# Kernel tuning notes

Measured on AMD Instinct MI355X. Metric: run time of the kernel, lower is better.

Reference implementation:

```python
import jax, jax.numpy as jnp
import numpy as np

N_NODES = 100000
N_EDGES = 1600000
IN_CH, HID, OUT_CH = 512, 32, 64


def setup_inputs() -> dict:
    key = jax.random.key(0)
    ks = jax.random.split(key, 8)
    x = jax.random.normal(ks[0], (N_NODES, IN_CH), dtype=jnp.float32)
    edge_index = jax.random.randint(ks[1], (2, N_EDGES), 0, N_NODES, dtype=jnp.int64)
    def glorot(k, fan_in, fan_out):
        lim = np.sqrt(6.0 / (fan_in + fan_out)).astype(np.float32)
        return jax.random.uniform(k, (fan_in, fan_out), jnp.float32, -lim, lim)
    return {
        "x": x,
        "edge_index": edge_index,
        "W1": glorot(ks[2], IN_CH, HID), "b1": jnp.zeros((HID,), jnp.float32),
        "W2": glorot(ks[3], HID, HID),   "b2": jnp.zeros((HID,), jnp.float32),
        "W3": glorot(ks[4], HID, OUT_CH),"b3": jnp.zeros((OUT_CH,), jnp.float32),
    }


def _gcn_norm(edge_index, n_nodes):
    # PyG GCNConv: add self-loops, symmetric normalization D^-1/2 (A+I) D^-1/2
    loops = jnp.arange(n_nodes, dtype=edge_index.dtype)
    src = jnp.concatenate([edge_index[0], loops])
    dst = jnp.concatenate([edge_index[1], loops])
    deg = jax.ops.segment_sum(jnp.ones_like(dst, dtype=jnp.float32), dst,
                              num_segments=n_nodes)
    dinv = jnp.where(deg > 0, jax.lax.rsqrt(deg), 0.0)
    norm = dinv[src] * dinv[dst]  # [E + N]
    return src, dst, norm


def _gcn_conv(x, W, b, src, dst, norm, n_nodes):
    h = x @ W                                  # [N, F_out] dense GEMM
    msg = h[src] * norm[:, None]               # gather + scale over edges
    out = jax.ops.segment_sum(msg, dst, num_segments=n_nodes)  # scatter-add
    return out + b


def reference(x, edge_index, W1, b1, W2, b2, W3, b3):
    n = x.shape[0]
    src, dst, norm = _gcn_norm(edge_index, n)
    h = _gcn_conv(x, W1, b1, src, dst, norm, n)
    h = jax.nn.relu(h)  # dropout is identity in eval mode (training=False)
    h = _gcn_conv(h, W2, b2, src, dst, norm, n)
    h = jax.nn.relu(h)
    h = _gcn_conv(h, W3, b3, src, dst, norm, n)
    return jax.nn.log_softmax(h, axis=1)
```

## Files before the change

### kernel.cpp

```cpp
#include <hip/hip_runtime.h>
#include <math.h>

static constexpr int NN    = 100000;
static constexpr int NBUCK = (NN + 255) / 256;

#define CDIV(a,b) (((a)+(b)-1)/(b))

__device__ __forceinline__ float bf2f(unsigned short u) {
    return __uint_as_float(((unsigned)u) << 16);
}
__device__ __forceinline__ unsigned short f2bf(float f) {
    unsigned u = __float_as_uint(f);
    u += 0x7fffu + ((u >> 16) & 1u);
    return (unsigned short)(u >> 16);
}

__global__ __launch_bounds__(512) void k_zero(int* __restrict__ p, int n) {
    int i = blockIdx.x * 512 + threadIdx.x;
    if (i < n) p[i] = 0;
}

__global__ __launch_bounds__(256) void k_bcount(const int* __restrict__ dst,
                                                int* __restrict__ bcnt,
                                                int E, int chunk) {
    __shared__ int lc[NBUCK];
    for (int i = threadIdx.x; i < NBUCK; i += 256) lc[i] = 0;
    __syncthreads();
    int e0 = blockIdx.x * chunk;
    int e1 = e0 + chunk; if (e1 > E) e1 = E;
    for (int e = e0 + threadIdx.x; e < e1; e += 256)
        atomicAdd(&lc[dst[e] >> 8], 1);
    __syncthreads();
    for (int i = threadIdx.x; i < NBUCK; i += 256)
        if (lc[i]) atomicAdd(&bcnt[i], lc[i]);
}

__global__ __launch_bounds__(512) void k_bscan(const int* __restrict__ bcnt,
                                               int* __restrict__ bbase,
                                               int* __restrict__ bfill, int E) {
    __shared__ int sm[512];
    int t = threadIdx.x;
    int v = (t < NBUCK) ? bcnt[t] : 0;
    sm[t] = v; __syncthreads();
    for (int off = 1; off < 512; off <<= 1) {
        int u = (t >= off) ? sm[t - off] : 0;
        __syncthreads();
        sm[t] += u;
        __syncthreads();
    }
    if (t < NBUCK) { int ex = sm[t] - v; bbase[t] = ex; bfill[t] = ex; }
    if (t == 0) bbase[NBUCK] = E;
}

__global__ __launch_bounds__(256) void k_bpart(const int* __restrict__ src,
                                               const int* __restrict__ dst,
                                               int* __restrict__ bfill,
                                               unsigned int* __restrict__ part,
                                               int E, int chunk) {
    __shared__ int lc[NBUCK];
    __shared__ int boff[NBUCK];
    for (int i = threadIdx.x; i < NBUCK; i += 256) lc[i] = 0;
    __syncthreads();
    int e0 = blockIdx.x * chunk;
    int e1 = e0 + chunk; if (e1 > E) e1 = E;
    for (int e = e0 + threadIdx.x; e < e1; e += 256)
        atomicAdd(&lc[dst[e] >> 8], 1);
    __syncthreads();
    for (int i = threadIdx.x; i < NBUCK; i += 256) {
        int c = lc[i];
        boff[i] = c ? atomicAdd(&bfill[i], c) : 0;
        lc[i] = 0;
    }
    __syncthreads();
    for (int e = e0 + threadIdx.x; e < e1; e += 256) {
        int d = dst[e];
        int b = d >> 8;
        int pos = boff[b] + atomicAdd(&lc[b], 1);
        part[pos] = ((unsigned)src[e] << 8) | (unsigned)(d & 255);
    }
}

__global__ __launch_bounds__(256) void k_bbuild(const unsigned int* __restrict__ part,
                                                const int* __restrict__ bbase,
                                                int* __restrict__ row_ptr,
                                                float* __restrict__ dinv,
                                                int* __restrict__ col, int n, int E) {
    __shared__ int hist[256];
    __shared__ int excl[256];
    __shared__ int fill[256];
    const int b = blockIdx.x;
    const int t = threadIdx.x;
    const int e0 = bbase[b], e1 = bbase[b + 1];
    hist[t] = 0; fill[t] = 0;
    __syncthreads();
    for (int e = e0 + t; e < e1; e += 256)
        atomicAdd(&hist[part[e] & 255], 1);
    __syncthreads();
    int v = hist[t];
    excl[t] = v; __syncthreads();
    for (int off = 1; off < 256; off <<= 1) {
        int u = (t >= off) ? excl[t - off] : 0;
        __syncthreads();
        excl[t] += u;
        __syncthreads();
    }
    int ex = excl[t] - v;
    int g = b * 256 + t;
    if (g < n) {
        row_ptr[g] = e0 + ex;
        dinv[g] = rsqrtf((float)(v + 1));
    }
    if (b == 0 && t == 0) row_ptr[n] = E;
    excl[t] = e0 + ex;
    __syncthreads();
    for (int e = e0 + t; e < e1; e += 256) {
        unsigned u = part[e];
        int ld = u & 255;
        int pos = excl[ld] + atomicAdd(&fill[ld], 1);
        col[pos] = (int)(u >> 8);
    }
}

__global__ __launch_bounds__(256) void k_gemm1(const float* __restrict__ X,
                                               const float* __restrict__ W,
                                               const float* __restrict__ dinv,
                                               unsigned short* __restrict__ OUT,
                                               int nrows) {
    constexpr int K    = 512;
    constexpr int NOUT = 32;
    constexpr int KC   = 32;
    constexpr int RPB  = 64;
    constexpr int XST  = KC + 4;
    __shared__ float xs[2][RPB][XST];
    __shared__ float ws[2][KC][NOUT];

    const int t     = threadIdx.x;
    const int c0    = (t % 8) * 4;
    const int slot  = t / 8;
    const int grow0 = blockIdx.x * RPB;
    const int srow  = t / 8;
    const int skq   = t % 8;

    float acc[2][4] = {{0.f,0.f,0.f,0.f},{0.f,0.f,0.f,0.f}};

    auto clampRow = [&](int lrow) {
        int rr = grow0 + lrow;
        return (rr > nrows - 1) ? (nrows - 1) : rr;
    };
    const float* xrowA = X + (size_t)clampRow(srow) * K;
    const float* xrowB = X + (size_t)clampRow(32 + srow) * K;

    {
        float4 a = *(const float4*)&xrowA[skq * 4];
        float4 b = *(const float4*)&xrowB[skq * 4];
        float4 w = *(const float4*)&W[(size_t)srow * NOUT + skq * 4];
        *(float4*)&xs[0][srow][skq * 4]      = a;
        *(float4*)&xs[0][32 + srow][skq * 4] = b;
        *(float4*)&ws[0][srow][skq * 4]      = w;
    }
    __syncthreads();

    int buf = 0;
    const int r0 = slot * 2;
    for (int kc = 0; kc < K; kc += KC) {
        const bool more = (kc + KC < K);
        float4 pa, pb, pw;
        if (more) {
            pa = *(const float4*)&xrowA[kc + KC + skq * 4];
            pb = *(const float4*)&xrowB[kc + KC + skq * 4];
            pw = *(const float4*)&W[(size_t)(kc + KC + srow) * NOUT + skq * 4];
        }
        #pragma unroll
        for (int k = 0; k < KC; k += 4) {
            float4 x0 = *(const float4*)&xs[buf][r0][k];
            float4 x1 = *(const float4*)&xs[buf][r0 + 1][k];
            float4 w0 = *(const float4*)&ws[buf][k + 0][c0];
            float4 w1 = *(const float4*)&ws[buf][k + 1][c0];
            float4 w2 = *(const float4*)&ws[buf][k + 2][c0];
            float4 w3 = *(const float4*)&ws[buf][k + 3][c0];
            acc[0][0] += x0.x*w0.x + x0.y*w1.x + x0.z*w2.x + x0.w*w3.x;
            acc[0][1] += x0.x*w0.y + x0.y*w1.y + x0.z*w2.y + x0.w*w3.y;
            acc[0][2] += x0.x*w0.z + x0.y*w1.z + x0.z*w2.z + x0.w*w3.z;
            acc[0][3] += x0.x*w0.w + x0.y*w1.w + x0.z*w2.w + x0.w*w3.w;
            acc[1][0] += x1.x*w0.x + x1.y*w1.x + x1.z*w2.x + x1.w*w3.x;
            acc[1][1] += x1.x*w0.y + x1.y*w1.y + x1.z*w2.y + x1.w*w3.y;
            acc[1][2] += x1.x*w0.z + x1.y*w1.z + x1.z*w2.z + x1.w*w3.z;
            acc[1][3] += x1.x*w0.w + x1.y*w1.w + x1.z*w2.w + x1.w*w3.w;
        }
        if (more) {
            *(float4*)&xs[buf ^ 1][srow][skq * 4]      = pa;
            *(float4*)&xs[buf ^ 1][32 + srow][skq * 4] = pb;
            *(float4*)&ws[buf ^ 1][srow][skq * 4]      = pw;
            __syncthreads();
            buf ^= 1;
        }
    }
    #pragma unroll
    for (int r = 0; r < 2; r++) {
        int rr = grow0 + r0 + r;
        if (rr < nrows) {
            float d = dinv[rr];
            ushort4 o;
            o.x = f2bf(acc[r][0] * d); o.y = f2bf(acc[r][1] * d);
            o.z = f2bf(acc[r][2] * d); o.w = f2bf(acc[r][3] * d);
            *(ushort4*)&OUT[(size_t)rr * NOUT + c0] = o;
        }
    }
}

__device__ __forceinline__ float4 agg_gather_bf16(const unsigned short* __restrict__ HS,
                                                  const int* __restrict__ col,
                                                  int s0, int s1, int node, int c0) {
    float4 a0 = {0,0,0,0}, a1 = {0,0,0,0}, a2 = {0,0,0,0}, a3 = {0,0,0,0};
    int e = s0;
    for (; e + 3 < s1; e += 4) {
        int sA = col[e], sB = col[e + 1], sC = col[e + 2], sD = col[e + 3];
        ushort4 uA = *(const ushort4*)&HS[(size_t)sA * 32 + c0];
        ushort4 uB = *(const ushort4*)&HS[(size_t)sB * 32 + c0];
        ushort4 uC = *(const ushort4*)&HS[(size_t)sC * 32 + c0];
        ushort4 uD = *(const ushort4*)&HS[(size_t)sD * 32 + c0];
        a0.x += bf2f(uA.x); a0.y += bf2f(uA.y); a0.z += bf2f(uA.z); a0.w += bf2f(uA.w);
        a1.x += bf2f(uB.x); a1.y += bf2f(uB.y); a1.z += bf2f(uB.z); a1.w += bf2f(uB.w);
        a2.x += bf2f(uC.x); a2.y += bf2f(uC.y); a2.z += bf2f(uC.z); a2.w += bf2f(uC.w);
        a3.x += bf2f(uD.x); a3.y += bf2f(uD.y); a3.z += bf2f(uD.z); a3.w += bf2f(uD.w);
    }
    for (; e < s1; e++) {
        int sA = col[e];
        ushort4 uA = *(const ushort4*)&HS[(size_t)sA * 32 + c0];
        a0.x += bf2f(uA.x); a0.y += bf2f(uA.y); a0.z += bf2f(uA.z); a0.w += bf2f(uA.w);
    }
    ushort4 uS = *(const ushort4*)&HS[(size_t)node * 32 + c0];
    float4 acc;
    acc.x = a0.x + a1.x + a2.x + a3.x + bf2f(uS.x);
    acc.y = a0.y + a1.y + a2.y + a3.y + bf2f(uS.y);
    acc.z = a0.z + a1.z + a2.z + a3.z + bf2f(uS.z);
    acc.w = a0.w + a1.w + a2.w + a3.w + bf2f(uS.w);
    return acc;
}

__global__ __launch_bounds__(256) void k_fuse32(const unsigned short* __restrict__ HS,
                                                const int* __restrict__ row_ptr,
                                                const int* __restrict__ col,
                                                const float* __restrict__ dinv,
                                                const float* __restrict__ bin,
                                                const float* __restrict__ W,
                                                unsigned short* __restrict__ OUT, int n) {
    __shared__ float ws[32][32];
    {
        int i = threadIdx.x;
        int r = i / 8, c = (i % 8) * 4;
        *(float4*)&ws[r][c] = *(const float4*)&W[r * 32 + c];
    }
    __syncthreads();
    const int t    = threadIdx.x;
    const int node = blockIdx.x * 32 + t / 8;
    const int c0   = (t % 8) * 4;
    if (node >= n) return;
    const int s0 = row_ptr[node], s1 = row_ptr[node + 1];
    float4 acc = agg_gather_bf16(HS, col, s0, s1, node, c0);
    const float di = dinv[node];
    float4 b4 = *(const float4*)&bin[c0];
    float4 a;
    a.x = fmaxf(di * acc.x + b4.x, 0.f);
    a.y = fmaxf(di * acc.y + b4.y, 0.f);
    a.z = fmaxf(di * acc.z + b4.z, 0.f);
    a.w = fmaxf(di * acc.w + b4.w, 0.f);
    float4 o = {0,0,0,0};
    const int gb = (t & 63) & ~7;
    #pragma unroll
    for (int s = 0; s < 8; s++) {
        float4 as;
        as.x = __shfl(a.x, gb + s, 64);
        as.y = __shfl(a.y, gb + s, 64);
        as.z = __shfl(a.z, gb + s, 64);
        as.w = __shfl(a.w, gb + s, 64);
        const int k0 = s * 4;
        float4 w0 = *(const float4*)&ws[k0 + 0][c0];
        float4 w1 = *(const float4*)&ws[k0 + 1][c0];
        float4 w2 = *(const float4*)&ws[k0 + 2][c0];
        float4 w3 = *(const float4*)&ws[k0 + 3][c0];
        o.x += as.x*w0.x + as.y*w1.x + as.z*w2.x + as.w*w3.x;
        o.y += as.x*w0.y + as.y*w1.y + as.z*w2.y + as.w*w3.y;
        o.z += as.x*w0.z + as.y*w1.z + as.z*w2.z + as.w*w3.z;
        o.w += as.x*w0.w + as.y*w1.w + as.z*w2.w + as.w*w3.w;
    }
    ushort4 st;
    st.x = f2bf(o.x * di); st.y = f2bf(o.y * di);
    st.z = f2bf(o.z * di); st.w = f2bf(o.w * di);
    *(ushort4*)&OUT[(size_t)node * 32 + c0] = st;
}

__global__ __launch_bounds__(256) void k_aggscale(const unsigned short* __restrict__ HS,
                                                  const int* __restrict__ row_ptr,
                                                  const int* __restrict__ col,
                                                  const float* __restrict__ dinv,
                                                  const float* __restrict__ bin,
                                                  unsigned short* __restrict__ OUT, int n) {
    const int t    = threadIdx.x;
    const int node = blockIdx.x * 32 + t / 8;
    const int c0   = (t % 8) * 4;
    if (node >= n) return;
    const int s0 = row_ptr[node], s1 = row_ptr[node + 1];
    float4 acc = agg_gather_bf16(HS, col, s0, s1, node, c0);
    const float di = dinv[node];
    float4 b4 = *(const float4*)&bin[c0];
    ushort4 o;
    o.x = f2bf(di * fmaxf(di * acc.x + b4.x, 0.f));
    o.y = f2bf(di * fmaxf(di * acc.y + b4.y, 0.f));
    o.z = f2bf(di * fmaxf(di * acc.z + b4.z, 0.f));
    o.w = f2bf(di * fmaxf(di * acc.w + b4.w, 0.f));
    *(ushort4*)&OUT[(size_t)node * 32 + c0] = o;
}

__global__ __launch_bounds__(256) void k_fuseC(const unsigned short* __restrict__ YS,
                                               const int* __restrict__ row_ptr,
                                               const int* __restrict__ col,
                                               const float* __restrict__ dinv,
                                               const float* __restrict__ b3,
                                               const float* __restrict__ W,
                                               float* __restrict__ OUT, int n) {
    __shared__ float ws[32][64];
    {
        int i = threadIdx.x;
        int r0w = i / 16, cw = (i % 16) * 4;
        *(float4*)&ws[r0w][cw]      = *(const float4*)&W[r0w * 64 + cw];
        *(float4*)&ws[r0w + 16][cw] = *(const float4*)&W[(r0w + 16) * 64 + cw];
    }
    __syncthreads();
    const int t    = threadIdx.x;
    const int node = blockIdx.x * 32 + t / 8;
    const int c0   = (t % 8) * 4;
    if (node >= n) return;
    const int s0 = row_ptr[node], s1 = row_ptr[node + 1];
    float4 acc = agg_gather_bf16(YS, col, s0, s1, node, c0);
    const float di = dinv[node];
    float4 g;
    g.x = di * acc.x; g.y = di * acc.y; g.z = di * acc.z; g.w = di * acc.w;
    float4 oL = {0,0,0,0}, oH = {0,0,0,0};
    const int gb = (t & 63) & ~7;
    #pragma unroll
    for (int s = 0; s < 8; s++) {
        float4 gs;
        gs.x = __shfl(g.x, gb + s, 64);
        gs.y = __shfl(g.y, gb + s, 64);
        gs.z = __shfl(g.z, gb + s, 64);
        gs.w = __shfl(g.w, gb + s, 64);
        const int k0 = s * 4;
        #pragma unroll
        for (int q = 0; q < 4; q++) {
            float gv = (q == 0) ? gs.x : (q == 1) ? gs.y : (q == 2) ? gs.z : gs.w;
            float4 wL = *(const float4*)&ws[k0 + q][c0];
            float4 wH = *(const float4*)&ws[k0 + q][32 + c0];
            oL.x += gv * wL.x; oL.y += gv * wL.y; oL.z += gv * wL.z; oL.w += gv * wL.w;
            oH.x += gv * wH.x; oH.y += gv * wH.y; oH.z += gv * wH.z; oH.w += gv * wH.w;
        }
    }
    float4 bL = *(const float4*)&b3[c0];
    float4 bH = *(const float4*)&b3[32 + c0];
    oL.x += bL.x; oL.y += bL.y; oL.z += bL.z; oL.w += bL.w;
    oH.x += bH.x; oH.y += bH.y; oH.z += bH.z; oH.w += bH.w;
    float m = fmaxf(fmaxf(fmaxf(oL.x, oL.y), fmaxf(oL.z, oL.w)),
                    fmaxf(fmaxf(oH.x, oH.y), fmaxf(oH.z, oH.w)));
    #pragma unroll
    for (int off = 1; off < 8; off <<= 1) m = fmaxf(m, __shfl_xor(m, off, 64));
    float sum = expf(oL.x - m) + expf(oL.y - m) + expf(oL.z - m) + expf(oL.w - m)
              + expf(oH.x - m) + expf(oH.y - m) + expf(oH.z - m) + expf(oH.w - m);
    #pragma unroll
    for (int off = 1; off < 8; off <<= 1) sum += __shfl_xor(sum, off, 64);
    float lse = m + logf(sum);
    float4 rL, rH;
    rL.x = oL.x - lse; rL.y = oL.y - lse; rL.z = oL.z - lse; rL.w = oL.w - lse;
    rH.x = oH.x - lse; rH.y = oH.y - lse; rH.z = oH.z - lse; rH.w = oH.w - lse;
    *(float4*)&OUT[(size_t)node * 64 + c0]      = rL;
    *(float4*)&OUT[(size_t)node * 64 + 32 + c0] = rH;
}

extern "C" void kernel_launch(void* const* d_in, const int* in_sizes, int n_in,
                              void* d_out, int out_size, void* d_ws, size_t ws_size,
                              hipStream_t stream) {
    const float* x  = (const float*)d_in[0];
    const int*   ei = (const int*)d_in[1];
    const float* W1 = (const float*)d_in[2];
    const float* b1 = (const float*)d_in[3];
    const float* W2 = (const float*)d_in[4];
    const float* b2 = (const float*)d_in[5];
    const float* W3 = (const float*)d_in[6];
    const float* b3 = (const float*)d_in[7];
    float* out = (float*)d_out;

    const int E = in_sizes[1] / 2;
    const int n = NN;
    const int* src = ei;
    const int* dst = ei + E;

    char* p = (char*)d_ws;
    auto alloc = [&](size_t bytes) -> void* {
        void* r = p;
        p += (bytes + 63) & ~(size_t)63;
        return r;
    };
    int*            bcnt    = (int*)alloc((size_t)NBUCK * 4);
    int*            bbase   = (int*)alloc((size_t)(NBUCK + 1) * 4);
    int*            bfill   = (int*)alloc((size_t)NBUCK * 4);
    unsigned*       part    = (unsigned*)alloc((size_t)E * 4);
    int*            row_ptr = (int*)alloc((size_t)(n + 1) * 4);
    int*            col     = (int*)alloc((size_t)E * 4);
    float*          dinv    = (float*)alloc((size_t)n * 4);
    unsigned short* hs1     = (unsigned short*)alloc((size_t)n * 32 * 2);
    unsigned short* hs2     = (unsigned short*)alloc((size_t)n * 32 * 2);

    const int NBLK_A = 256;
    const int chunk  = CDIV(E, NBLK_A);

    k_zero<<<1, 512, 0, stream>>>(bcnt, NBUCK);
    k_bcount<<<NBLK_A, 256, 0, stream>>>(dst, bcnt, E, chunk);
    k_bscan<<<1, 512, 0, stream>>>(bcnt, bbase, bfill, E);
    k_bpart<<<NBLK_A, 256, 0, stream>>>(src, dst, bfill, part, E, chunk);
    k_bbuild<<<NBUCK, 256, 0, stream>>>(part, bbase, row_ptr, dinv, col, n, E);

    k_gemm1<<<CDIV(n, 64), 256, 0, stream>>>(x, W1, dinv, hs1, n);
    k_fuse32<<<CDIV(n, 32), 256, 0, stream>>>(hs1, row_ptr, col, dinv, b1, W2, hs2, n);
    k_aggscale<<<CDIV(n, 32), 256, 0, stream>>>(hs2, row_ptr, col, dinv, b2, hs1, n);
    k_fuseC<<<CDIV(n, 32), 256, 0, stream>>>(hs1, row_ptr, col, dinv, b3, W3, out, n);
}
```

Baseline: 223.2 us.

## Use direct global-to-LDS loads in GEMM1 and 16-byte gathers in aggregation

The first GEMM now stages X and W tiles with global_load_lds straight into shared memory. It drops the register round-trip and the padded stride, and uses an XOR-style rotated column swizzle to avoid bank conflicts. The three aggregation kernels switch from 4 lanes of 8-byte bf16 loads per node to 4 threads per node each doing 16-byte gathers. This halves the lanes per node and doubles the nodes per block. The aim is fewer memory instructions per gathered row and less staging overhead, at the cost of more registers per thread and a swizzle that must match the LDS write pattern exactly.

After: 233.5 us. 4.6% more time.

```diff
diff --git a/kernel.cpp b/kernel.cpp
--- a/kernel.cpp
+++ b/kernel.cpp
@@ -6,13 +6,13 @@
 
 #define CDIV(a,b) (((a)+(b)-1)/(b))
 
-__device__ __forceinline__ float bf2f(unsigned short u) {
-    return __uint_as_float(((unsigned)u) << 16);
-}
 __device__ __forceinline__ unsigned short f2bf(float f) {
     unsigned u = __float_as_uint(f);
     u += 0x7fffu + ((u >> 16) & 1u);
     return (unsigned short)(u >> 16);
+}
+__device__ __forceinline__ unsigned packbf(float lo, float hi) {
+    return (unsigned)f2bf(lo) | ((unsigned)f2bf(hi) << 16);
 }
 
 __global__ __launch_bounds__(512) void k_zero(int* __restrict__ p, int n) {
@@ -130,8 +130,7 @@
     constexpr int NOUT = 32;
     constexpr int KC   = 32;
     constexpr int RPB  = 64;
-    constexpr int XST  = KC + 4;
-    __shared__ float xs[2][RPB][XST];
+    __shared__ float xs[2][RPB][KC];
     __shared__ float ws[2][KC][NOUT];
 
     const int t     = threadIdx.x;
@@ -140,6 +139,7 @@
     const int grow0 = blockIdx.x * RPB;
     const int srow  = t / 8;
     const int skq   = t % 8;
+    const int wid8  = (t >> 6) * 8;
 
     float acc[2][4] = {{0.f,0.f,0.f,0.f},{0.f,0.f,0.f,0.f}};
 
@@ -147,33 +147,36 @@
         int rr = grow0 + lrow;
         return (rr > nrows - 1) ? (nrows - 1) : rr;
     };
-    const float* xrowA = X + (size_t)clampRow(srow) * K;
-    const float* xrowB = X + (size_t)clampRow(32 + srow) * K;
-
-    {
-        float4 a = *(const float4*)&xrowA[skq * 4];
-        float4 b = *(const float4*)&xrowB[skq * 4];
-        float4 w = *(const float4*)&W[(size_t)srow * NOUT + skq * 4];
-        *(float4*)&xs[0][srow][skq * 4]      = a;
-        *(float4*)&xs[0][32 + srow][skq * 4] = b;
-        *(float4*)&ws[0][srow][skq * 4]      = w;
-    }
+    const int scol = ((skq - ((srow >> 1) & 7)) & 7) * 4;
+    const float* xrowA = X + (size_t)clampRow(srow) * K + scol;
+    const float* xrowB = X + (size_t)clampRow(32 + srow) * K + scol;
+
+    auto stage = [&](int bf, int kc) {
+        __builtin_amdgcn_global_load_lds(
+            (const __attribute__((address_space(1))) void*)(xrowA + kc),
+            (__attribute__((address_space(3))) void*)&xs[bf][wid8][0], 16, 0, 0);
+        __builtin_amdgcn_global_load_lds(
+            (const __attribute__((address_space(1))) void*)(xrowB + kc),
+            (__attribute__((address_space(3))) void*)&xs[bf][32 + wid8][0], 16, 0, 0);
+        __builtin_amdgcn_global_load_lds(
+            (const __attribute__((address_space(1))) void*)(W + (size_t)(kc + srow) * NOUT + skq * 4),
+            (__attribute__((address_space(3))) void*)&ws[bf][wid8][0], 16, 0, 0);
+    };
+
+    stage(0, 0);
     __syncthreads();
 
     int buf = 0;
     const int r0 = slot * 2;
+    const int q4 = (slot & 7) * 4;
     for (int kc = 0; kc < K; kc += KC) {
         const bool more = (kc + KC < K);
-        float4 pa, pb, pw;
-        if (more) {
-            pa = *(const float4*)&xrowA[kc + KC + skq * 4];
-            pb = *(const float4*)&xrowB[kc + KC + skq * 4];
-            pw = *(const float4*)&W[(size_t)(kc + KC + srow) * NOUT + skq * 4];
-        }
+        if (more) stage(buf ^ 1, kc + KC);
         #pragma unroll
         for (int k = 0; k < KC; k += 4) {
-            float4 x0 = *(const float4*)&xs[buf][r0][k];
-            float4 x1 = *(const float4*)&xs[buf][r0 + 1][k];
+            const int kq = (k + q4) & 31;
+            float4 x0 = *(const float4*)&xs[buf][r0][kq];
+            float4 x1 = *(const float4*)&xs[buf][r0 + 1][kq];
             float4 w0 = *(const float4*)&ws[buf][k + 0][c0];
             float4 w1 = *(const float4*)&ws[buf][k + 1][c0];
             float4 w2 = *(const float4*)&ws[buf][k + 2][c0];
@@ -187,13 +190,8 @@
             acc[1][2] += x1.x*w0.z + x1.y*w1.z + x1.z*w2.z + x1.w*w3.z;
             acc[1][3] += x1.x*w0.w + x1.y*w1.w + x1.z*w2.w + x1.w*w3.w;
         }
-        if (more) {
-            *(float4*)&xs[buf ^ 1][srow][skq * 4]      = pa;
-            *(float4*)&xs[buf ^ 1][32 + srow][skq * 4] = pb;
-            *(float4*)&ws[buf ^ 1][srow][skq * 4]      = pw;
-            __syncthreads();
-            buf ^= 1;
-        }
+        __syncthreads();
+        if (more) buf ^= 1;
     }
     #pragma unroll
     for (int r = 0; r < 2; r++) {
@@ -208,34 +206,42 @@
     }
 }
 
-__device__ __forceinline__ float4 agg_gather_bf16(const unsigned short* __restrict__ HS,
-                                                  const int* __restrict__ col,
-                                                  int s0, int s1, int node, int c0) {
-    float4 a0 = {0,0,0,0}, a1 = {0,0,0,0}, a2 = {0,0,0,0}, a3 = {0,0,0,0};
+__device__ __forceinline__ void acc8(float* a, uint4 u) {
+    a[0] += __uint_as_float(u.x << 16);
+    a[1] += __uint_as_float(u.x & 0xffff0000u);
+    a[2] += __uint_as_float(u.y << 16);
+    a[3] += __uint_as_float(u.y & 0xffff0000u);
+    a[4] += __uint_as_float(u.z << 16);
+    a[5] += __uint_as_float(u.z & 0xffff0000u);
+    a[6] += __uint_as_float(u.w << 16);
+    a[7] += __uint_as_float(u.w & 0xffff0000u);
+}
+
+__device__ __forceinline__ void agg_gather8(const unsigned short* __restrict__ HS,
+                                            const int* __restrict__ col,
+                                            int s0, int s1, int node, int c0h,
+                                            float* __restrict__ out) {
+    float a0[8], a1[8], a2[8], a3[8];
+    #pragma unroll
+    for (int j = 0; j < 8; j++) { a0[j] = a1[j] = a2[j] = a3[j] = 0.f; }
+    const char* base = (const char*)HS + (size_t)c0h * 2;
     int e = s0;
     for (; e + 3 < s1; e += 4) {
         int sA = col[e], sB = col[e + 1], sC = col[e + 2], sD = col[e + 3];
-        ushort4 uA = *(const ushort4*)&HS[(size_t)sA * 32 + c0];
-        ushort4 uB = *(const ushort4*)&HS[(size_t)sB * 32 + c0];
-        ushort4 uC = *(const ushort4*)&HS[(size_t)sC * 32 + c0];
-        ushort4 uD = *(const ushort4*)&HS[(size_t)sD * 32 + c0];
-        a0.x += bf2f(uA.x); a0.y += bf2f(uA.y); a0.z += bf2f(uA.z); a0.w += bf2f(uA.w);
-        a1.x += bf2f(uB.x); a1.y += bf2f(uB.y); a1.z += bf2f(uB.z); a1.w += bf2f(uB.w);
-        a2.x += bf2f(uC.x); a2.y += bf2f(uC.y); a2.z += bf2f(uC.z); a2.w += bf2f(uC.w);
-        a3.x += bf2f(uD.x); a3.y += bf2f(uD.y); a3.z += bf2f(uD.z); a3.w += bf2f(uD.w);
+        uint4 uA = *(const uint4*)(base + (size_t)sA * 64);
+        uint4 uB = *(const uint4*)(base + (size_t)sB * 64);
+        uint4 uC = *(const uint4*)(base + (size_t)sC * 64);
+        uint4 uD = *(const uint4*)(base + (size_t)sD * 64);
+        acc8(a0, uA); acc8(a1, uB); acc8(a2, uC); acc8(a3, uD);
     }
     for (; e < s1; e++) {
-        int sA = col[e];
-        ushort4 uA = *(const ushort4*)&HS[(size_t)sA * 32 + c0];
-        a0.x += bf2f(uA.x); a0.y += bf2f(uA.y); a0.z += bf2f(uA.z); a0.w += bf2f(uA.w);
-    }
-    ushort4 uS = *(const ushort4*)&HS[(size_t)node * 32 + c0];
-    float4 acc;
-    acc.x = a0.x + a1.x + a2.x + a3.x + bf2f(uS.x);
-    acc.y = a0.y + a1.y + a2.y + a3.y + bf2f(uS.y);
-    acc.z = a0.z + a1.z + a2.z + a3.z + bf2f(uS.z);
-    acc.w = a0.w + a1.w + a2.w + a3.w + bf2f(uS.w);
-    return acc;
+        uint4 uA = *(const uint4*)(base + (size_t)col[e] * 64);
+        acc8(a0, uA);
+    }
+    uint4 uS = *(const uint4*)(base + (size_t)node * 64);
+    acc8(a1, uS);
+    #pragma unroll
+    for (int j = 0; j < 8; j++) out[j] = (a0[j] + a1[j]) + (a2[j] + a3[j]);
 }
 
 __global__ __launch_bounds__(256) void k_fuse32(const unsigned short* __restrict__ HS,
@@ -253,41 +259,37 @@
     }
     __syncthreads();
     const int t    = threadIdx.x;
-    const int node = blockIdx.x * 32 + t / 8;
-    const int c0   = (t % 8) * 4;
+    const int node = blockIdx.x * 64 + t / 4;
+    const int c0h  = (t % 4) * 8;
     if (node >= n) return;
     const int s0 = row_ptr[node], s1 = row_ptr[node + 1];
-    float4 acc = agg_gather_bf16(HS, col, s0, s1, node, c0);
+    float acc[8];
+    agg_gather8(HS, col, s0, s1, node, c0h, acc);
     const float di = dinv[node];
-    float4 b4 = *(const float4*)&bin[c0];
-    float4 a;
-    a.x = fmaxf(di * acc.x + b4.x, 0.f);
-    a.y = fmaxf(di * acc.y + b4.y, 0.f);
-    a.z = fmaxf(di * acc.z + b4.z, 0.f);
-    a.w = fmaxf(di * acc.w + b4.w, 0.f);
-    float4 o = {0,0,0,0};
-    const int gb = (t & 63) & ~7;
-    #pragma unroll
-    for (int s = 0; s < 8; s++) {
-        float4 as;
-        as.x = __shfl(a.x, gb + s, 64);
-        as.y = __shfl(a.y, gb + s, 64);
-        as.z = __shfl(a.z, gb + s, 64);
-        as.w = __shfl(a.w, gb + s, 64);
-        const int k0 = s * 4;
-        float4 w0 = *(const float4*)&ws[k0 + 0][c0];
-        float4 w1 = *(const float4*)&ws[k0 + 1][c0];
-        float4 w2 = *(const float4*)&ws[k0 + 2][c0];
-        float4 w3 = *(const float4*)&ws[k0 + 3][c0];
-        o.x += as.x*w0.x + as.y*w1.x + as.z*w2.x + as.w*w3.x;
-        o.y += as.x*w0.y + as.y*w1.y + as.z*w2.y + as.w*w3.y;
-        o.z += as.x*w0.z + as.y*w1.z + as.z*w2.z + as.w*w3.z;
-        o.w += as.x*w0.w + as.y*w1.w + as.z*w2.w + as.w*w3.w;
-    }
-    ushort4 st;
-    st.x = f2bf(o.x * di); st.y = f2bf(o.y * di);
-    st.z = f2bf(o.z * di); st.w = f2bf(o.w * di);
-    *(ushort4*)&OUT[(size_t)node * 32 + c0] = st;
+    float a[8];
+    #pragma unroll
+    for (int j = 0; j < 8; j++)
+        a[j] = fmaxf(di * acc[j] + bin[c0h + j], 0.f);
+    float o[8] = {0,0,0,0,0,0,0,0};
+    const int gb = (t & 63) & ~3;
+    #pragma unroll
+    for (int s = 0; s < 4; s++) {
+        #pragma unroll
+        for (int j = 0; j < 8; j++) {
+            float av = __shfl(a[j], gb + s, 64);
+            const int kr = s * 8 + j;
+            float4 w0 = *(const float4*)&ws[kr][c0h];
+            float4 w1 = *(const float4*)&ws[kr][c0h + 4];
+            o[0] += av * w0.x; o[1] += av * w0.y; o[2] += av * w0.z; o[3] += av * w0.w;
+            o[4] += av * w1.x; o[5] += av * w1.y; o[6] += av * w1.z; o[7] += av * w1.w;
+        }
+    }
+    uint4 st;
+    st.x = packbf(o[0] * di, o[1] * di);
+    st.y = packbf(o[2] * di, o[3] * di);
+    st.z = packbf(o[4] * di, o[5] * di);
+    st.w = packbf(o[6] * di, o[7] * di);
+    *(uint4*)&OUT[(size_t)node * 32 + c0h] = st;
 }
 
 __global__ __launch_bounds__(256) void k_aggscale(const unsigned short* __restrict__ HS,
@@ -297,19 +299,23 @@
                                                   const float* __restrict__ bin,
                                                   unsigned short* __restrict__ OUT, int n) {
     const int t    = threadIdx.x;
-    const int node = blockIdx.x * 32 + t / 8;
-    const int c0   = (t % 8) * 4;
+    const int node = blockIdx.x * 64 + t / 4;
+    const int c0h  = (t % 4) * 8;
     if (node >= n) return;
     const int s0 = row_ptr[node], s1 = row_ptr[node + 1];
-    float4 acc = agg_gather_bf16(HS, col, s0, s1, node, c0);
+    float acc[8];
+    agg_gather8(HS, col, s0, s1, node, c0h, acc);
     const float di = dinv[node];
-    float4 b4 = *(const float4*)&bin[c0];
-    ushort4 o;
-    o.x = f2bf(di * fmaxf(di * acc.x + b4.x, 0.f));
-    o.y = f2bf(di * fmaxf(di * acc.y + b4.y, 0.f));
-    o.z = f2bf(di * fmaxf(di * acc.z + b4.z, 0.f));
-    o.w = f2bf(di * fmaxf(di * acc.w + b4.w, 0.f));
-    *(ushort4*)&OUT[(size_t)node * 32 + c0] = o;
+    float o[8];
+    #pragma unroll
+    for (int j = 0; j < 8; j++)
+        o[j] = di * fmaxf(di * acc[j] + bin[c0h + j], 0.f);
+    uint4 st;
+    st.x = packbf(o[0], o[1]);
+    st.y = packbf(o[2], o[3]);
+    st.z = packbf(o[4], o[5]);
+    st.w = packbf(o[6], o[7]);
+    *(uint4*)&OUT[(size_t)node * 32 + c0h] = st;
 }
 
 __global__ __launch_bounds__(256) void k_fuseC(const unsigned short* __restrict__ YS,
@@ -328,51 +334,58 @@
     }
     __syncthreads();
     const int t    = threadIdx.x;
-    const int node = blockIdx.x * 32 + t / 8;
-    const int c0   = (t % 8) * 4;
+    const int node = blockIdx.x * 64 + t / 4;
+    const int c0h  = (t % 4) * 8;
+    const int c0f  = (t % 4) * 16;
     if (node >= n) return;
     const int s0 = row_ptr[node], s1 = row_ptr[node + 1];
-    float4 acc = agg_gather_bf16(YS, col, s0, s1, node, c0);
+    float acc[8];
+    agg_gather8(YS, col, s0, s1, node, c0h, acc);
     const float di = dinv[node];
-    float4 g;
-    g.x = di * acc.x; g.y = di * acc.y; g.z = di * acc.z; g.w = di * acc.w;
-    float4 oL = {0,0,0,0}, oH = {0,0,0,0};
-    const int gb = (t & 63) & ~7;
-    #pragma unroll
-    for (int s = 0; s < 8; s++) {
-        float4 gs;
-        gs.x = __shfl(g.x, gb + s, 64);
-        gs.y = __shfl(g.y, gb + s, 64);
-        gs.z = __shfl(g.z, gb + s, 64);
-        gs.w = __shfl(g.w, gb + s, 64);
-        const int k0 = s * 4;
+    float g[8];
+    #pragma unroll
+    for (int j = 0; j < 8; j++) g[j] = di * acc[j];
+    float o[16];
+    #pragma unroll
+    for (int j = 0; j < 16; j++) o[j] = b3[c0f + j];
+    const int gb = (t & 63) & ~3;
+    #pragma unroll
+    for (int s = 0; s < 4; s++) {
         #pragma unroll
-        for (int q = 0; q < 4; q++) {
-            float gv = (q == 0) ? gs.x : (q == 1) ? gs.y : (q == 2) ? gs.z : gs.w;
-            float4 wL = *(const float4*)&ws[k0 + q][c0];
-            float4 wH = *(const float4*)&ws[k0 + q][32 + c0];
-            oL.x += gv * wL.x; oL.y += gv * wL.y; oL.z += gv * wL.z; oL.w += gv * wL.w;
-            oH.x += gv * wH.x; oH.y += gv * wH.y; oH.z += gv * wH.z; oH.w += gv * wH.w;
+        for (int j = 0; j < 8; j++) {
+            float gv = __shfl(g[j], gb + s, 64);
+            const int kr = s * 8 + j;
+            float4 w0 = *(const float4*)&ws[kr][c0f];
+            float4 w1 = *(const float4*)&ws[kr][c0f + 4];
+            float4 w2 = *(const float4*)&ws[kr][c0f + 8];
+            float4 w3 = *(const float4*)&ws[kr][c0f + 12];
+            o[0]  += gv * w0.x; o[1]  += gv * w0.y; o[2]  += gv * w0.z; o[3]  += gv * w0.w;
+            o[4]  += gv * w1.x; o[5]  += gv * w1.y; o[6]  += gv * w1.z; o[7]  += gv * w1.w;
+            o[8]  += gv * w2.x; o[9]  += gv * w2.y; o[10] += gv * w2.z; o[11] += gv * w2.w;
+            o[12] += gv * w3.x; o[13] += gv * w3.y; o[14] += gv * w3.z; o[15] += gv * w3.w;
         }
     }
-    float4 bL = *(const float4*)&b3[c0];
-    float4 bH = *(const float4*)&b3[32 + c0];
-    oL.x += bL.x; oL.y += bL.y; oL.z += bL.z; oL.w += bL.w;
-    oH.x += bH.x; oH.y += bH.y; oH.z += bH.z; oH.w += bH.w;
-    float m = fmaxf(fmaxf(fmaxf(oL.x, oL.y), fmaxf(oL.z, oL.w)),
-                    fmaxf(fmaxf(oH.x, oH.y), fmaxf(oH.z, oH.w)));
-    #pragma unroll
-    for (int off = 1; off < 8; off <<= 1) m = fmaxf(m, __shfl_xor(m, off, 64));
-    float sum = expf(oL.x - m) + expf(oL.y - m) + expf(oL.z - m) + expf(oL.w - m)
-              + expf(oH.x - m) + expf(oH.y - m) + expf(oH.z - m) + expf(oH.w - m);
-    #pragma unroll
-    for (int off = 1; off < 8; off <<= 1) sum += __shfl_xor(sum, off, 64);
+    float m = o[0];
+    #pragma unroll
+    for (int j = 1; j < 16; j++) m = fmaxf(m, o[j]);
+    #pragma unroll
+    for (int off = 1; off < 4; off <<= 1) m = fmaxf(m, __shfl_xor(m, off, 64));
+    float sum = 0.f;
+    #pragma unroll
+    for (int j = 0; j < 16; j++) sum += expf(o[j] - m);
+    #pragma unroll
+    for (int off = 1; off < 4; off <<= 1) sum += __shfl_xor(sum, off, 64);
     float lse = m + logf(sum);
-    float4 rL, rH;
-    rL.x = oL.x - lse; rL.y = oL.y - lse; rL.z = oL.z - lse; rL.w = oL.w - lse;
-    rH.x = oH.x - lse; rH.y = oH.y - lse; rH.z = oH.z - lse; rH.w = oH.w - lse;
-    *(float4*)&OUT[(size_t)node * 64 + c0]      = rL;
-    *(float4*)&OUT[(size_t)node * 64 + 32 + c0] = rH;
+    float4 r0v, r1v, r2v, r3v;
+    r0v.x = o[0] - lse;  r0v.y = o[1] - lse;  r0v.z = o[2] - lse;  r0v.w = o[3] - lse;
+    r1v.x = o[4] - lse;  r1v.y = o[5] - lse;  r1v.z = o[6] - lse;  r1v.w = o[7] - lse;
+    r2v.x = o[8] - lse;  r2v.y = o[9] - lse;  r2v.z = o[10] - lse; r2v.w = o[11] - lse;
+    r3v.x = o[12] - lse; r3v.y = o[13] - lse; r3v.z = o[14] - lse; r3v.w = o[15] - lse;
+    float* ob = &OUT[(size_t)node * 64 + c0f];
+    *(float4*)&ob[0]  = r0v;
+    *(float4*)&ob[4]  = r1v;
+    *(float4*)&ob[8]  = r2v;
+    *(float4*)&ob[12] = r3v;
 }
 
 extern "C" void kernel_launch(void* const* d_in, const int* in_sizes, int n_in,
@@ -419,7 +432,7 @@
     k_bbuild<<<NBUCK, 256, 0, stream>>>(part, bbase, row_ptr, dinv, col, n, E);
 
     k_gemm1<<<CDIV(n, 64), 256, 0, stream>>>(x, W1, dinv, hs1, n);
-    k_fuse32<<<CDIV(n, 32), 256, 0, stream>>>(hs1, row_ptr, col, dinv, b1, W2, hs2, n);
-    k_aggscale<<<CDIV(n, 32), 256, 0, stream>>>(hs2, row_ptr, col, dinv, b2, hs1, n);
-    k_fuseC<<<CDIV(n, 32), 256, 0, stream>>>(hs1, row_ptr, col, dinv, b3, W3, out, n);
-}
+    k_fuse32<<<CDIV(n, 64), 256, 0, stream>>>(hs1, row_ptr, col, dinv, b1, W2, hs2, n);
+    k_aggscale<<<CDIV(n, 64), 256, 0, stream>>>(hs2, row_ptr, col, dinv, b2, hs1, n);
+    k_fuseC<<<CDIV(n, 64), 256, 0, stream>>>(hs1, row_ptr, col, dinv, b3, W3, out, n);
+}
```

## Use bf16 MFMA for first-layer GEMM with pre-transposed swizzled weights

Applied to the files above, without the earlier changes.

Rewrites the 100000x512x32 GEMM to convert X rows to bf16 on the fly and compute with 16x16x32 bf16 MFMA instructions. A new small kernel converts W1 once per call into a transposed, XOR-swizzled bf16 layout that each block copies into LDS. This replaces the FP32 FMA path and its double-buffered X staging, and aims to make the memory-bound X read the only real cost. It lowers the precision of the GEMM inputs to bf16 and adds one extra launch.

New measurement: 185.4 us. 1.2x faster.

```diff
diff --git a/kernel.cpp b/kernel.cpp
--- a/kernel.cpp
+++ b/kernel.cpp
@@ -5,6 +5,9 @@
 static constexpr int NBUCK = (NN + 255) / 256;
 
 #define CDIV(a,b) (((a)+(b)-1)/(b))
+
+typedef __attribute__((ext_vector_type(8))) short bf16x8;
+typedef __attribute__((ext_vector_type(4))) float f32x4;
 
 __device__ __forceinline__ float bf2f(unsigned short u) {
     return __uint_as_float(((unsigned)u) << 16);
@@ -18,6 +21,13 @@
 __global__ __launch_bounds__(512) void k_zero(int* __restrict__ p, int n) {
     int i = blockIdx.x * 512 + threadIdx.x;
     if (i < n) p[i] = 0;
+}
+
+__global__ __launch_bounds__(256) void k_wconv(const float* __restrict__ W,
+                                               unsigned short* __restrict__ WT) {
+    int i = blockIdx.x * 256 + threadIdx.x;
+    int k = i >> 5, c = i & 31;
+    WT[c * 512 + (((k >> 3) ^ (c & 7)) << 3) + (k & 7)] = f2bf(W[i]);
 }
 
 __global__ __launch_bounds__(256) void k_bcount(const int* __restrict__ dst,
@@ -122,88 +132,56 @@
 }
 
 __global__ __launch_bounds__(256) void k_gemm1(const float* __restrict__ X,
-                                               const float* __restrict__ W,
+                                               const unsigned short* __restrict__ WT,
                                                const float* __restrict__ dinv,
                                                unsigned short* __restrict__ OUT,
                                                int nrows) {
-    constexpr int K    = 512;
-    constexpr int NOUT = 32;
-    constexpr int KC   = 32;
-    constexpr int RPB  = 64;
-    constexpr int XST  = KC + 4;
-    __shared__ float xs[2][RPB][XST];
-    __shared__ float ws[2][KC][NOUT];
-
-    const int t     = threadIdx.x;
-    const int c0    = (t % 8) * 4;
-    const int slot  = t / 8;
-    const int grow0 = blockIdx.x * RPB;
-    const int srow  = t / 8;
-    const int skq   = t % 8;
-
-    float acc[2][4] = {{0.f,0.f,0.f,0.f},{0.f,0.f,0.f,0.f}};
-
-    auto clampRow = [&](int lrow) {
-        int rr = grow0 + lrow;
-        return (rr > nrows - 1) ? (nrows - 1) : rr;
-    };
-    const float* xrowA = X + (size_t)clampRow(srow) * K;
-    const float* xrowB = X + (size_t)clampRow(32 + srow) * K;
-
+    __shared__ unsigned short wt[32][512];
+    const int t = threadIdx.x;
     {
-        float4 a = *(const float4*)&xrowA[skq * 4];
-        float4 b = *(const float4*)&xrowB[skq * 4];
-        float4 w = *(const float4*)&W[(size_t)srow * NOUT + skq * 4];
-        *(float4*)&xs[0][srow][skq * 4]      = a;
-        *(float4*)&xs[0][32 + srow][skq * 4] = b;
-        *(float4*)&ws[0][srow][skq * 4]      = w;
-    }
-    __syncthreads();
-
-    int buf = 0;
-    const int r0 = slot * 2;
-    for (int kc = 0; kc < K; kc += KC) {
-        const bool more = (kc + KC < K);
-        float4 pa, pb, pw;
-        if (more) {
-            pa = *(const float4*)&xrowA[kc + KC + skq * 4];
-            pb = *(const float4*)&xrowB[kc + KC + skq * 4];
-            pw = *(const float4*)&W[(size_t)(kc + KC + srow) * NOUT + skq * 4];
-        }
+        const uint4* s = (const uint4*)WT;
+        uint4* d = (uint4*)&wt[0][0];
         #pragma unroll
-        for (int k = 0; k < KC; k += 4) {
-            float4 x0 = *(const float4*)&xs[buf][r0][k];
-            float4 x1 = *(const float4*)&xs[buf][r0 + 1][k];
-            float4 w0 = *(const float4*)&ws[buf][k + 0][c0];
-            float4 w1 = *(const float4*)&ws[buf][k + 1][c0];
-            float4 w2 = *(const float4*)&ws[buf][k + 2][c0];
-            float4 w3 = *(const float4*)&ws[buf][k + 3][c0];
-            acc[0][0] += x0.x*w0.x + x0.y*w1.x + x0.z*w2.x + x0.w*w3.x;
-            acc[0][1] += x0.x*w0.y + x0.y*w1.y + x0.z*w2.y + x0.w*w3.y;
-            acc[0][2] += x0.x*w0.z + x0.y*w1.z + x0.z*w2.z + x0.w*w3.z;
-            acc[0][3] += x0.x*w0.w + x0.y*w1.w + x0.z*w2.w + x0.w*w3.w;
-            acc[1][0] += x1.x*w0.x + x1.y*w1.x + x1.z*w2.x + x1.w*w3.x;
-            acc[1][1] += x1.x*w0.y + x1.y*w1.y + x1.z*w2.y + x1.w*w3.y;
-            acc[1][2] += x1.x*w0.z + x1.y*w1.z + x1.z*w2.z + x1.w*w3.z;
-            acc[1][3] += x1.x*w0.w + x1.y*w1.w + x1.z*w2.w + x1.w*w3.w;
-        }
-        if (more) {
-            *(float4*)&xs[buf ^ 1][srow][skq * 4]      = pa;
-            *(float4*)&xs[buf ^ 1][32 + srow][skq * 4] = pb;
-            *(float4*)&ws[buf ^ 1][srow][skq * 4]      = pw;
-            __syncthreads();
-            buf ^= 1;
-        }
+        for (int i = 0; i < 8; i++) d[t + 256 * i] = s[t + 256 * i];
+    }
+    __syncthreads();
+
+    const int lane  = t & 63;
+    const int w     = t >> 6;
+    const int grow0 = blockIdx.x * 64 + w * 16;
+    const int m     = lane & 15;
+    const int kb    = lane >> 4;
+    int row = grow0 + m; if (row > nrows - 1) row = nrows - 1;
+    const float* xrow = X + (size_t)row * 512 + kb * 8;
+
+    f32x4 acc0 = {0.f, 0.f, 0.f, 0.f};
+    f32x4 acc1 = {0.f, 0.f, 0.f, 0.f};
+    const int mx  = m & 7;
+    const unsigned short* wrow0 = &wt[m][0];
+    const unsigned short* wrow1 = &wt[m + 16][0];
+
+    #pragma unroll 4
+    for (int kk = 0; kk < 512; kk += 32) {
+        float4 xa = *(const float4*)(xrow + kk);
+        float4 xb = *(const float4*)(xrow + kk + 4);
+        bf16x8 a;
+        a[0] = (short)f2bf(xa.x); a[1] = (short)f2bf(xa.y);
+        a[2] = (short)f2bf(xa.z); a[3] = (short)f2bf(xa.w);
+        a[4] = (short)f2bf(xb.x); a[5] = (short)f2bf(xb.y);
+        a[6] = (short)f2bf(xb.z); a[7] = (short)f2bf(xb.w);
+        const int g = (kk >> 3) + kb;
+        bf16x8 b0 = *(const bf16x8*)&wrow0[((g ^ mx) & 63) * 8];
+        bf16x8 b1 = *(const bf16x8*)&wrow1[((g ^ mx) & 63) * 8];
+        acc0 = __builtin_amdgcn_mfma_f32_16x16x32_bf16(a, b0, acc0, 0, 0, 0);
+        acc1 = __builtin_amdgcn_mfma_f32_16x16x32_bf16(a, b1, acc1, 0, 0, 0);
     }
     #pragma unroll
-    for (int r = 0; r < 2; r++) {
-        int rr = grow0 + r0 + r;
+    for (int j = 0; j < 4; j++) {
+        int rr = grow0 + kb * 4 + j;
         if (rr < nrows) {
             float d = dinv[rr];
-            ushort4 o;
-            o.x = f2bf(acc[r][0] * d); o.y = f2bf(acc[r][1] * d);
-            o.z = f2bf(acc[r][2] * d); o.w = f2bf(acc[r][3] * d);
-            *(ushort4*)&OUT[(size_t)rr * NOUT + c0] = o;
+            OUT[(size_t)rr * 32 + m]      = f2bf(acc0[j] * d);
+            OUT[(size_t)rr * 32 + 16 + m] = f2bf(acc1[j] * d);
         }
     }
 }
@@ -406,6 +384,7 @@
     int*            row_ptr = (int*)alloc((size_t)(n + 1) * 4);
     int*            col     = (int*)alloc((size_t)E * 4);
     float*          dinv    = (float*)alloc((size_t)n * 4);
+    unsigned short* wtbf    = (unsigned short*)alloc((size_t)512 * 32 * 2);
     unsigned short* hs1     = (unsigned short*)alloc((size_t)n * 32 * 2);
     unsigned short* hs2     = (unsigned short*)alloc((size_t)n * 32 * 2);
 
@@ -413,12 +392,13 @@
     const int chunk  = CDIV(E, NBLK_A);
 
     k_zero<<<1, 512, 0, stream>>>(bcnt, NBUCK);
+    k_wconv<<<64, 256, 0, stream>>>(W1, wtbf);
     k_bcount<<<NBLK_A, 256, 0, stream>>>(dst, bcnt, E, chunk);
     k_bscan<<<1, 512, 0, stream>>>(bcnt, bbase, bfill, E);
     k_bpart<<<NBLK_A, 256, 0, stream>>>(src, dst, bfill, part, E, chunk);
     k_bbuild<<<NBUCK, 256, 0, stream>>>(part, bbase, row_ptr, dinv, col, n, E);
 
-    k_gemm1<<<CDIV(n, 64), 256, 0, stream>>>(x, W1, dinv, hs1, n);
+    k_gemm1<<<CDIV(n, 64), 256, 0, stream>>>(x, wtbf, dinv, hs1, n);
     k_fuse32<<<CDIV(n, 32), 256, 0, stream>>>(hs1, row_ptr, col, dinv, b1, W2, hs2, n);
     k_aggscale<<<CDIV(n, 32), 256, 0, stream>>>(hs2, row_ptr, col, dinv, b2, hs1, n);
     k_fuseC<<<CDIV(n, 32), 256, 0, stream>>>(hs1, row_ptr, col, dinv, b3, W3, out, n);
```
